# Performance work log

Hardware: AMD Instinct MI355X
Metric: run time of the kernel (lower is better)

Reference implementation:

```python
import jax, jax.numpy as jnp
import numpy as np

N, H, W = 128, 400, 400          # instances, feature canvas
MS = 28                          # mask_size = pooler_resolution*2
CT, CS = 80, 53                  # thing / stuff classes
STRIDE = 4                       # common_stride
HG, WG = 1600, 1600              # image-resolution gt panoptic
IGNORE = 255
LOSS_W = 1.0


def setup_inputs() -> dict:
    key = jax.random.key(0)
    ks = jax.random.split(key, 8)
    mask_logits = jax.random.normal(ks[0], (N, CT, MS, MS), jnp.float32)
    stuff_logit = jax.random.normal(ks[1], (CS, H, W), jnp.float32)
    thing_logit = jax.random.normal(ks[2], (CT, H, W), jnp.float32)
    # valid boxes in image pixel coords (x0,y0,x2,y2), width/height >= 16 px
    x0 = jax.random.uniform(ks[3], (N,), minval=0.0, maxval=1200.0)
    y0 = jax.random.uniform(ks[4], (N,), minval=0.0, maxval=1200.0)
    wh = jax.random.uniform(ks[5], (N, 2), minval=16.0, maxval=400.0)
    x2 = jnp.minimum(x0 + wh[:, 0], WG - 1.0)
    y2 = jnp.minimum(y0 + wh[:, 1], HG - 1.0)
    bbox = jnp.stack([x0, y0, x2, y2], axis=1).astype(jnp.float32)
    cls_idx = jax.random.randint(ks[6], (N,), 0, CT, dtype=jnp.int32)
    gt_panoptic = jax.random.randint(ks[7], (HG, WG), 0, CS + N, dtype=jnp.int32)
    return {"mask_logits": mask_logits, "stuff_logit": stuff_logit,
            "thing_logit": thing_logit, "bbox": bbox, "cls_idx": cls_idx,
            "gt_panoptic": gt_panoptic}


def _axis_sample(lo, size, grid, src_size):
    """Bilinear sampling coords along one axis (align_corners=False).
    lo: [N] box start (feat px, int); size: [N] box extent; grid: [G].
    Returns (idx0, idx1, frac) each [N, G]."""
    dst = grid[None, :].astype(jnp.float32) - lo[:, None].astype(jnp.float32)
    src = (dst + 0.5) * (src_size / size[:, None].astype(jnp.float32)) - 0.5
    f = jnp.floor(src)
    t = src - f
    i0 = jnp.clip(f, 0, src_size - 1).astype(jnp.int32)
    i1 = jnp.clip(f + 1, 0, src_size - 1).astype(jnp.int32)
    return i0, i1, t


def reference(mask_logits, stuff_logit, thing_logit, bbox, cls_idx, gt_panoptic):
    # _separate_fetch_logits: gather per-instance class channel -> [N, MS, MS]
    ml = mask_logits[jnp.arange(N), cls_idx]

    # _unmap_mask_logit_single: boxes -> feat coords (.long() == floor, boxes >= 0)
    bl = jnp.floor(bbox / STRIDE).astype(jnp.int32)
    x0b, y0b, x2b, y2b = bl[:, 0], bl[:, 1], bl[:, 2], bl[:, 3]
    hh = y2b - y0b + 1
    ww = x2b - x0b + 1
    ys = jnp.arange(H, dtype=jnp.int32)
    xs = jnp.arange(W, dtype=jnp.int32)

    i0, i1, ty = _axis_sample(y0b, hh, ys, MS)   # [N, H]
    j0, j1, tx = _axis_sample(x0b, ww, xs, MS)   # [N, W]

    # separable bilinear: rows [N, H, MS] then cols [N, H, W]
    r0 = jnp.take_along_axis(ml, jnp.broadcast_to(i0[:, :, None], (N, H, MS)), axis=1)
    r1 = jnp.take_along_axis(ml, jnp.broadcast_to(i1[:, :, None], (N, H, MS)), axis=1)
    rows = r0 * (1.0 - ty)[:, :, None] + r1 * ty[:, :, None]
    c0 = jnp.take_along_axis(rows, jnp.broadcast_to(j0[:, None, :], (N, H, W)), axis=2)
    c1 = jnp.take_along_axis(rows, jnp.broadcast_to(j1[:, None, :], (N, H, W)), axis=2)
    val = c0 * (1.0 - tx)[:, None, :] + c1 * tx[:, None, :]

    vy = (ys[None, :] >= jnp.maximum(y0b, 0)[:, None]) & (ys[None, :] <= jnp.minimum(y2b, H - 1)[:, None])
    vx = (xs[None, :] >= jnp.maximum(x0b, 0)[:, None]) & (xs[None, :] <= jnp.minimum(x2b, W - 1)[:, None])
    thing_mask_logit = jnp.where(vy[:, :, None] & vx[:, None, :], val, 0.0)

    # _crop_thing_logit_single: int()/round() based crop window
    bf = bbox / STRIDE
    cx1 = bf[:, 0].astype(jnp.int32)
    cy1 = bf[:, 1].astype(jnp.int32)
    cx2 = (jnp.round(bf[:, 2]) + 1.0).astype(jnp.int32)
    cy2 = (jnp.round(bf[:, 3]) + 1.0).astype(jnp.int32)
    my = (ys[None, :] >= cy1[:, None]) & (ys[None, :] < cy2[:, None])
    mx = (xs[None, :] >= cx1[:, None]) & (xs[None, :] < cx2[:, None])
    thing_sem_logit = jnp.where(my[:, :, None] & mx[:, None, :], thing_logit[cls_idx], 0.0)

    pan_logit = jnp.concatenate(
        [stuff_logit[None], (thing_mask_logit + thing_sem_logit)[None]], axis=1)

    # gt nearest-downsample to feat_size, then CE with ignore_index
    iy = jnp.floor(jnp.arange(H) * (HG / H)).astype(jnp.int32)
    ix = jnp.floor(jnp.arange(W) * (WG / W)).astype(jnp.int32)
    gt_ds = gt_panoptic[iy[:, None], ix[None, :]][None]          # [1, H, W]
    logp = jax.nn.log_softmax(pan_logit, axis=1)
    tgt = jnp.clip(gt_ds, 0, CS + N - 1)
    nll = -jnp.take_along_axis(logp, tgt[:, None], axis=1)[:, 0]  # [1, H, W]
    valid = gt_ds != IGNORE
    pan_loss = LOSS_W * jnp.sum(jnp.where(valid, nll, 0.0)) / jnp.maximum(
        jnp.sum(valid).astype(jnp.float32), 1.0)
    return pan_logit, pan_loss
```

## Files before the change

kernel.cpp:

```cpp
#include <hip/hip_runtime.h>
#include <math.h>

#define N_   128
#define H_   400
#define W_   400
#define MS_  28
#define CT_  80
#define CS_  53
#define HW_  (H_*W_)
#define NCH_ (CS_ + N_)
#define WG_  1600
#define IGN_ 255
#define G_   8
#define CPG_ 23
#define PPT_ 4
#define BT_  256
#define PPB_ (BT_*PPT_)
#define GX_  ((HW_ + PPB_ - 1)/PPB_)

typedef float f4 __attribute__((ext_vector_type(4)));
typedef unsigned long long u64;

struct NParam {
  int vy_lo, vy_hi, vx_lo, vx_hi;
  int cy1, cy2, cx1, cx2;
  float sy, sx;
  int y0b, x0b;
  int mlbase, thbase;
  int pad0, pad1;
};

__device__ unsigned int g_tdone[GX_];
__device__ unsigned int g_done;
__device__ u64          g_lp2[(G_*HW_)/2];
__device__ float        g_vt[HW_];
__device__ float        g_part[GX_*2];

static __device__ __forceinline__ u64 pack2(float a, float b) {
  union { float f[2]; u64 u; } t; t.f[0] = a; t.f[1] = b; return t.u;
}
static __device__ __forceinline__ void unpack2(u64 u, float& a, float& b) {
  union { float f[2]; u64 u; } t; t.u = u; a = t.f[0]; b = t.f[1];
}
#define AG_ST(p, v) __hip_atomic_store((p), (v), __ATOMIC_RELAXED, __HIP_MEMORY_SCOPE_AGENT)
#define AG_LD(p)    __hip_atomic_load((p), __ATOMIC_RELAXED, __HIP_MEMORY_SCOPE_AGENT)

__device__ __forceinline__ void lse_update(float v, float& m, float& s) {
  float d = v - m;
  float e = __expf(-fabsf(d));
  s = (d > 0.0f) ? fmaf(s, e, 1.0f) : (s + e);
  m = fmaxf(m, v);
}

__global__ __launch_bounds__(256) void main_kernel(
    const float* __restrict__ mask_logits,
    const float* __restrict__ stuff_logit,
    const float* __restrict__ thing_logit,
    const float* __restrict__ bbox,
    const int*   __restrict__ cls_idx,
    const int*   __restrict__ gt,
    float* __restrict__ out)
{
  __shared__ NParam spar[N_];
  __shared__ int4   sbox[N_];
  __shared__ float  red[8];
  __shared__ unsigned s_tick, s_fin;
  int tid = threadIdx.x;
  if (tid < N_) {
    int n = tid;
    float b0 = bbox[4*n+0]*0.25f, b1 = bbox[4*n+1]*0.25f,
          b2 = bbox[4*n+2]*0.25f, b3 = bbox[4*n+3]*0.25f;
    int x0b = (int)floorf(b0), y0b = (int)floorf(b1);
    int x2b = (int)floorf(b2), y2b = (int)floorf(b3);
    int hh = y2b - y0b + 1, ww = x2b - x0b + 1;
    NParam p;
    p.vy_lo = max(y0b, 0); p.vy_hi = min(y2b, H_-1);
    p.vx_lo = max(x0b, 0); p.vx_hi = min(x2b, W_-1);
    p.cy1 = (int)b1; p.cx1 = (int)b0;
    p.cy2 = (int)(rintf(b3) + 1.0f);
    p.cx2 = (int)(rintf(b2) + 1.0f);
    p.sy = 28.0f / (float)hh; p.sx = 28.0f / (float)ww;
    p.y0b = y0b; p.x0b = x0b;
    int cls = cls_idx[n];
    p.mlbase = (n*CT_ + cls)*(MS_*MS_);
    p.thbase = cls*HW_;
    p.pad0 = 0; p.pad1 = 0;
    spar[n] = p;
    sbox[n] = make_int4(min(p.vy_lo, p.cy1), max(p.vy_hi, p.cy2 - 1),
                        min(p.vx_lo, p.cx1), max(p.vx_hi, p.cx2 - 1));
  }
  __syncthreads();

  int pix0 = (blockIdx.x*BT_ + tid)*PPT_;
  bool act = (pix0 < HW_);
  int grp = blockIdx.y;
  int c0 = grp*CPG_;
  int c1 = min(NCH_, c0 + CPG_);

  int y = 0, xb = 0;
  int graw[PPT_];
  #pragma unroll
  for (int k = 0; k < PPT_; ++k) graw[k] = IGN_;

  if (act) {
    y  = pix0 / W_;
    xb = pix0 - y*W_;

    int tcs[PPT_];
    #pragma unroll
    for (int k = 0; k < PPT_; ++k) {
      int g = gt[y*(4*WG_) + (xb + k)*4];
      graw[k] = g;
      tcs[k] = min(max(g, 0), NCH_-1);
    }

    float mv[PPT_], sv[PPT_], vts[PPT_];
    #pragma unroll
    for (int k = 0; k < PPT_; ++k) { mv[k] = -INFINITY; sv[k] = 0.0f; vts[k] = 0.0f; }
    int zc = 0;

    int c = c0;
    for (; c < min(c1, CS_); ++c) {
      f4 v = *(const f4*)(stuff_logit + c*HW_ + pix0);
      *(f4*)(out + c*HW_ + pix0) = v;
      #pragma unroll
      for (int k = 0; k < PPT_; ++k) {
        lse_update(v[k], mv[k], sv[k]);
        if (c == tcs[k]) vts[k] = v[k];
      }
    }
    for (; c < c1; ++c) {
      int n = c - CS_;
      int4 u = sbox[n];
      bool rej = (y < u.x) | (y > u.y) | (xb > u.w) | (xb + PPT_ - 1 < u.z);
      if (__all(rej)) {
        f4 z = {0.0f, 0.0f, 0.0f, 0.0f};
        *(f4*)(out + c*HW_ + pix0) = z;
        ++zc;
        continue;
      }
      NParam p = spar[n];
      float vv[PPT_] = {0.0f, 0.0f, 0.0f, 0.0f};
      if (y >= p.cy1 && y < p.cy2 && xb < p.cx2 && xb+PPT_-1 >= p.cx1) {
        f4 t = *(const f4*)(thing_logit + p.thbase + pix0);
        #pragma unroll
        for (int k = 0; k < PPT_; ++k) {
          int x = xb + k;
          if (x >= p.cx1 && x < p.cx2) vv[k] = t[k];
        }
      }
      if (y >= p.vy_lo && y <= p.vy_hi && xb <= p.vx_hi && xb+PPT_-1 >= p.vx_lo) {
        float srcy = ((float)(y - p.y0b) + 0.5f)*p.sy - 0.5f;
        float fy = floorf(srcy); float ty = srcy - fy;
        int i0 = (int)fminf(fmaxf(fy,        0.0f), (float)(MS_-1));
        int i1 = (int)fminf(fmaxf(fy + 1.0f, 0.0f), (float)(MS_-1));
        const float* r0p = mask_logits + p.mlbase + i0*MS_;
        const float* r1p = mask_logits + p.mlbase + i1*MS_;
        #pragma unroll
        for (int k = 0; k < PPT_; ++k) {
          int x = xb + k;
          if (x >= p.vx_lo && x <= p.vx_hi) {
            float srcx = ((float)(x - p.x0b) + 0.5f)*p.sx - 0.5f;
            float fx = floorf(srcx); float tx = srcx - fx;
            int j0 = (int)fminf(fmaxf(fx,        0.0f), (float)(MS_-1));
            int j1 = (int)fminf(fmaxf(fx + 1.0f, 0.0f), (float)(MS_-1));
            float r0 = r0p[j0]*(1.0f - tx) + r0p[j1]*tx;
            float r1 = r1p[j0]*(1.0f - tx) + r1p[j1]*tx;
            vv[k] += r0*(1.0f - ty) + r1*ty;
          }
        }
      }
      f4 ov = {vv[0], vv[1], vv[2], vv[3]};
      *(f4*)(out + c*HW_ + pix0) = ov;
      #pragma unroll
      for (int k = 0; k < PPT_; ++k) {
        lse_update(vv[k], mv[k], sv[k]);
        if (c == tcs[k]) vts[k] = vv[k];
      }
    }

    float zcf = (float)zc;
    float lpv[PPT_];
    #pragma unroll
    for (int k = 0; k < PPT_; ++k) {
      float m = mv[k], s = sv[k];
      if (zc > 0) {
        if (m >= 0.0f) { s = fmaf(zcf, __expf(-m), s); }
        else           { s = fmaf(s, __expf(m), zcf); m = 0.0f; }
      }
      lpv[k] = m + __logf(s);
    }
    int base = (grp*HW_ + pix0) >> 1;
    AG_ST(&g_lp2[base],     pack2(lpv[0], lpv[1]));
    AG_ST(&g_lp2[base + 1], pack2(lpv[2], lpv[3]));
    #pragma unroll
    for (int k = 0; k < PPT_; ++k)
      if (tcs[k] >= c0 && tcs[k] < c1) AG_ST(&g_vt[pix0 + k], vts[k]);
  }

  __syncthreads();
  if (tid == 0)
    s_tick = __hip_atomic_fetch_add(&g_tdone[blockIdx.x], 1u,
                                    __ATOMIC_RELAXED, __HIP_MEMORY_SCOPE_AGENT);
  __syncthreads();
  if ((s_tick & (unsigned)(G_-1)) != (unsigned)(G_-1)) return;

  float nll = 0.0f, cnt = 0.0f;
  if (act) {
    float m2[PPT_], s2[PPT_];
    {
      u64 a = AG_LD(&g_lp2[pix0 >> 1]);
      u64 b = AG_LD(&g_lp2[(pix0 >> 1) + 1]);
      unpack2(a, m2[0], m2[1]); unpack2(b, m2[2], m2[3]);
      #pragma unroll
      for (int k = 0; k < PPT_; ++k) s2[k] = 1.0f;
    }
    #pragma unroll
    for (int g = 1; g < G_; ++g) {
      int base = (g*HW_ + pix0) >> 1;
      u64 a = AG_LD(&g_lp2[base]);
      u64 b = AG_LD(&g_lp2[base + 1]);
      float lg[PPT_];
      unpack2(a, lg[0], lg[1]); unpack2(b, lg[2], lg[3]);
      #pragma unroll
      for (int k = 0; k < PPT_; ++k) {
        float d = lg[k] - m2[k];
        float e = __expf(-fabsf(d));
        s2[k] = (d > 0.0f) ? fmaf(s2[k], e, 1.0f) : (s2[k] + e);
        m2[k] = fmaxf(m2[k], lg[k]);
      }
    }
    #pragma unroll
    for (int k = 0; k < PPT_; ++k) {
      float vt = AG_LD(&g_vt[pix0 + k]);
      bool valid = (graw[k] != IGN_);
      nll += valid ? (m2[k] + __logf(s2[k]) - vt) : 0.0f;
      cnt += valid ? 1.0f : 0.0f;
    }
  }

  for (int off = 32; off >= 1; off >>= 1) {
    nll += __shfl_down(nll, off, 64);
    cnt += __shfl_down(cnt, off, 64);
  }
  int lane = tid & 63, wid = tid >> 6;
  if (lane == 0) { red[wid*2] = nll; red[wid*2+1] = cnt; }
  __syncthreads();
  if (tid == 0) {
    float ts  = red[0] + red[2] + red[4] + red[6];
    float tcn = red[1] + red[3] + red[5] + red[7];
    AG_ST(&g_part[blockIdx.x*2],     ts);
    AG_ST(&g_part[blockIdx.x*2 + 1], tcn);
    asm volatile("s_waitcnt vmcnt(0)" ::: "memory");
    unsigned d = __hip_atomic_fetch_add(&g_done, 1u,
                                        __ATOMIC_RELAXED, __HIP_MEMORY_SCOPE_AGENT);
    s_fin = ((d % (unsigned)GX_) == (unsigned)(GX_-1)) ? 1u : 0u;
  }
  __syncthreads();
  if (s_fin) {
    float a = 0.0f, b = 0.0f;
    if (tid < GX_) {
      a = AG_LD(&g_part[tid*2]);
      b = AG_LD(&g_part[tid*2 + 1]);
    }
    for (int off = 32; off >= 1; off >>= 1) {
      a += __shfl_down(a, off, 64);
      b += __shfl_down(b, off, 64);
    }
    if (lane == 0) { red[wid*2] = a; red[wid*2+1] = b; }
    __syncthreads();
    if (tid == 0) {
      float ts  = red[0] + red[2] + red[4] + red[6];
      float tcn = red[1] + red[3] + red[5] + red[7];
      out[NCH_*HW_] = ts / fmaxf(tcn, 1.0f);
    }
  }
}

extern "C" void kernel_launch(void* const* d_in, const int* in_sizes, int n_in,
                              void* d_out, int out_size, void* d_ws, size_t ws_size,
                              hipStream_t stream) {
  const float* mask_logits = (const float*)d_in[0];
  const float* stuff_logit = (const float*)d_in[1];
  const float* thing_logit = (const float*)d_in[2];
  const float* bbox        = (const float*)d_in[3];
  const int*   cls_idx     = (const int*)d_in[4];
  const int*   gt          = (const int*)d_in[5];
  float* out = (float*)d_out;

  dim3 grid1(GX_, G_);
  main_kernel<<<grid1, BT_, 0, stream>>>(mask_logits, stuff_logit, thing_logit,
                                         bbox, cls_idx, gt, out);
}
```

Measured before the change: 220.2 us.

## Drop channel-group split; each thread handles all channels for two pixels

Removes the 8-way channel-group grid dimension along with its global logsumexp partials and per-tile ticket merge. Each thread now walks all 181 channels for 2 pixels, computing the log-softmax and NLL directly in registers. This eliminates the g_lp2/g_vt round trips and the second merge phase. In exchange the grid gets smaller and each thread runs a longer serial channel loop with narrower float2 accesses, which may cut memory-level parallelism. The final reduction now loops over twice as many partials.

```diff
diff --git a/kernel.cpp b/kernel.cpp
--- a/kernel.cpp
+++ b/kernel.cpp
@@ -11,15 +11,12 @@
 #define NCH_ (CS_ + N_)
 #define WG_  1600
 #define IGN_ 255
-#define G_   8
-#define CPG_ 23
-#define PPT_ 4
+#define PPT_ 2
 #define BT_  256
 #define PPB_ (BT_*PPT_)
 #define GX_  ((HW_ + PPB_ - 1)/PPB_)
 
-typedef float f4 __attribute__((ext_vector_type(4)));
-typedef unsigned long long u64;
+typedef float f2 __attribute__((ext_vector_type(2)));
 
 struct NParam {
   int vy_lo, vy_hi, vx_lo, vx_hi;
@@ -30,18 +27,9 @@
   int pad0, pad1;
 };
 
-__device__ unsigned int g_tdone[GX_];
 __device__ unsigned int g_done;
-__device__ u64          g_lp2[(G_*HW_)/2];
-__device__ float        g_vt[HW_];
 __device__ float        g_part[GX_*2];
 
-static __device__ __forceinline__ u64 pack2(float a, float b) {
-  union { float f[2]; u64 u; } t; t.f[0] = a; t.f[1] = b; return t.u;
-}
-static __device__ __forceinline__ void unpack2(u64 u, float& a, float& b) {
-  union { float f[2]; u64 u; } t; t.u = u; a = t.f[0]; b = t.f[1];
-}
 #define AG_ST(p, v) __hip_atomic_store((p), (v), __ATOMIC_RELAXED, __HIP_MEMORY_SCOPE_AGENT)
 #define AG_LD(p)    __hip_atomic_load((p), __ATOMIC_RELAXED, __HIP_MEMORY_SCOPE_AGENT)
 
@@ -64,7 +52,7 @@
   __shared__ NParam spar[N_];
   __shared__ int4   sbox[N_];
   __shared__ float  red[8];
-  __shared__ unsigned s_tick, s_fin;
+  __shared__ unsigned s_fin;
   int tid = threadIdx.x;
   if (tid < N_) {
     int n = tid;
@@ -93,20 +81,13 @@
 
   int pix0 = (blockIdx.x*BT_ + tid)*PPT_;
   bool act = (pix0 < HW_);
-  int grp = blockIdx.y;
-  int c0 = grp*CPG_;
-  int c1 = min(NCH_, c0 + CPG_);
-
-  int y = 0, xb = 0;
-  int graw[PPT_];
-  #pragma unroll
-  for (int k = 0; k < PPT_; ++k) graw[k] = IGN_;
+  float nll = 0.0f, cnt = 0.0f;
 
   if (act) {
-    y  = pix0 / W_;
-    xb = pix0 - y*W_;
-
-    int tcs[PPT_];
+    int y  = pix0 / W_;
+    int xb = pix0 - y*W_;
+
+    int graw[PPT_], tcs[PPT_];
     #pragma unroll
     for (int k = 0; k < PPT_; ++k) {
       int g = gt[y*(4*WG_) + (xb + k)*4];
@@ -119,30 +100,29 @@
     for (int k = 0; k < PPT_; ++k) { mv[k] = -INFINITY; sv[k] = 0.0f; vts[k] = 0.0f; }
     int zc = 0;
 
-    int c = c0;
-    for (; c < min(c1, CS_); ++c) {
-      f4 v = *(const f4*)(stuff_logit + c*HW_ + pix0);
-      *(f4*)(out + c*HW_ + pix0) = v;
+    for (int c = 0; c < CS_; ++c) {
+      f2 v = *(const f2*)(stuff_logit + c*HW_ + pix0);
+      *(f2*)(out + c*HW_ + pix0) = v;
       #pragma unroll
       for (int k = 0; k < PPT_; ++k) {
         lse_update(v[k], mv[k], sv[k]);
         if (c == tcs[k]) vts[k] = v[k];
       }
     }
-    for (; c < c1; ++c) {
+    for (int c = CS_; c < NCH_; ++c) {
       int n = c - CS_;
       int4 u = sbox[n];
       bool rej = (y < u.x) | (y > u.y) | (xb > u.w) | (xb + PPT_ - 1 < u.z);
       if (__all(rej)) {
-        f4 z = {0.0f, 0.0f, 0.0f, 0.0f};
-        *(f4*)(out + c*HW_ + pix0) = z;
+        f2 z = {0.0f, 0.0f};
+        *(f2*)(out + c*HW_ + pix0) = z;
         ++zc;
         continue;
       }
       NParam p = spar[n];
-      float vv[PPT_] = {0.0f, 0.0f, 0.0f, 0.0f};
+      float vv[PPT_] = {0.0f, 0.0f};
       if (y >= p.cy1 && y < p.cy2 && xb < p.cx2 && xb+PPT_-1 >= p.cx1) {
-        f4 t = *(const f4*)(thing_logit + p.thbase + pix0);
+        f2 t = *(const f2*)(thing_logit + p.thbase + pix0);
         #pragma unroll
         for (int k = 0; k < PPT_; ++k) {
           int x = xb + k;
@@ -170,8 +150,8 @@
           }
         }
       }
-      f4 ov = {vv[0], vv[1], vv[2], vv[3]};
-      *(f4*)(out + c*HW_ + pix0) = ov;
+      f2 ov = {vv[0], vv[1]};
+      *(f2*)(out + c*HW_ + pix0) = ov;
       #pragma unroll
       for (int k = 0; k < PPT_; ++k) {
         lse_update(vv[k], mv[k], sv[k]);
@@ -180,7 +160,6 @@
     }
 
     float zcf = (float)zc;
-    float lpv[PPT_];
     #pragma unroll
     for (int k = 0; k < PPT_; ++k) {
       float m = mv[k], s = sv[k];
@@ -188,53 +167,8 @@
         if (m >= 0.0f) { s = fmaf(zcf, __expf(-m), s); }
         else           { s = fmaf(s, __expf(m), zcf); m = 0.0f; }
       }
-      lpv[k] = m + __logf(s);
-    }
-    int base = (grp*HW_ + pix0) >> 1;
-    AG_ST(&g_lp2[base],     pack2(lpv[0], lpv[1]));
-    AG_ST(&g_lp2[base + 1], pack2(lpv[2], lpv[3]));
-    #pragma unroll
-    for (int k = 0; k < PPT_; ++k)
-      if (tcs[k] >= c0 && tcs[k] < c1) AG_ST(&g_vt[pix0 + k], vts[k]);
-  }
-
-  __syncthreads();
-  if (tid == 0)
-    s_tick = __hip_atomic_fetch_add(&g_tdone[blockIdx.x], 1u,
-                                    __ATOMIC_RELAXED, __HIP_MEMORY_SCOPE_AGENT);
-  __syncthreads();
-  if ((s_tick & (unsigned)(G_-1)) != (unsigned)(G_-1)) return;
-
-  float nll = 0.0f, cnt = 0.0f;
-  if (act) {
-    float m2[PPT_], s2[PPT_];
-    {
-      u64 a = AG_LD(&g_lp2[pix0 >> 1]);
-      u64 b = AG_LD(&g_lp2[(pix0 >> 1) + 1]);
-      unpack2(a, m2[0], m2[1]); unpack2(b, m2[2], m2[3]);
-      #pragma unroll
-      for (int k = 0; k < PPT_; ++k) s2[k] = 1.0f;
-    }
-    #pragma unroll
-    for (int g = 1; g < G_; ++g) {
-      int base = (g*HW_ + pix0) >> 1;
-      u64 a = AG_LD(&g_lp2[base]);
-      u64 b = AG_LD(&g_lp2[base + 1]);
-      float lg[PPT_];
-      unpack2(a, lg[0], lg[1]); unpack2(b, lg[2], lg[3]);
-      #pragma unroll
-      for (int k = 0; k < PPT_; ++k) {
-        float d = lg[k] - m2[k];
-        float e = __expf(-fabsf(d));
-        s2[k] = (d > 0.0f) ? fmaf(s2[k], e, 1.0f) : (s2[k] + e);
-        m2[k] = fmaxf(m2[k], lg[k]);
-      }
-    }
-    #pragma unroll
-    for (int k = 0; k < PPT_; ++k) {
-      float vt = AG_LD(&g_vt[pix0 + k]);
       bool valid = (graw[k] != IGN_);
-      nll += valid ? (m2[k] + __logf(s2[k]) - vt) : 0.0f;
+      nll += valid ? (m + __logf(s) - vts[k]) : 0.0f;
       cnt += valid ? 1.0f : 0.0f;
     }
   }
@@ -259,10 +193,8 @@
   __syncthreads();
   if (s_fin) {
     float a = 0.0f, b = 0.0f;
-    if (tid < GX_) {
-      a = AG_LD(&g_part[tid*2]);
-      b = AG_LD(&g_part[tid*2 + 1]);
-    }
+    if (tid < GX_)        { a += AG_LD(&g_part[tid*2]);        b += AG_LD(&g_part[tid*2 + 1]); }
+    if (tid + BT_ < GX_)  { a += AG_LD(&g_part[(tid+BT_)*2]);  b += AG_LD(&g_part[(tid+BT_)*2 + 1]); }
     for (int off = 32; off >= 1; off >>= 1) {
       a += __shfl_down(a, off, 64);
       b += __shfl_down(b, off, 64);
@@ -288,7 +220,6 @@
   const int*   gt          = (const int*)d_in[5];
   float* out = (float*)d_out;
 
-  dim3 grid1(GX_, G_);
-  main_kernel<<<grid1, BT_, 0, stream>>>(mask_logits, stuff_logit, thing_logit,
-                                         bbox, cls_idx, gt, out);
+  main_kernel<<<GX_, BT_, 0, stream>>>(mask_logits, stuff_logit, thing_logit,
+                                       bbox, cls_idx, gt, out);
 }
```

Result: slower. 237.1 us (+7.7%).
